# Optimization experiments

Hardware: AMD Instinct MI355X
Metric: run time of the kernel (lower is better)

## Reference

```python
import jax, jax.numpy as jnp
import numpy as np

B = 4096
D = 68 * 68  # 4624
L = 68
E = 1024


def setup_inputs() -> dict:
    key = jax.random.key(0)
    ks = jax.random.split(key, 24)
    rn = lambda k, shape, scale: jax.random.normal(k, shape, dtype=jnp.float32) * scale
    inp = {
        "x": rn(ks[0], (B, D), 1.0),
        "eps": rn(ks[1], (B, L), 1.0),
        # weights scaled ~1/sqrt(fan_in) to avoid sigmoid saturation
        "fc11_w": rn(ks[2], (E, D), 1.0 / np.sqrt(D)),
        "fc11_b": rn(ks[3], (E,), 0.01),
        "fc12_w": rn(ks[4], (E, D), 1.0 / np.sqrt(D)),
        "fc12_b": rn(ks[5], (E,), 0.01),
        "fc21_w": rn(ks[6], (L, E), 1.0 / np.sqrt(E)),
        "fc21_b": rn(ks[7], (L,), 0.01),
        "fc22_w": rn(ks[8], (L, E), 1.0 / np.sqrt(E)),
        "fc22_b": rn(ks[9], (L,), 0.01),
        "W3": rn(ks[10], (5, L, L), 1.0 / np.sqrt(L)),
        "b3": rn(ks[11], (5, L), 0.01),
        "W4": rn(ks[12], (5, L, L), 1.0 / np.sqrt(L)),
        "b4": rn(ks[13], (5, L), 0.01),
        "W5": rn(ks[14], (3, L, L), 1.0 / np.sqrt(L)),
        "b5": rn(ks[15], (3, L), 0.01),
        "fc6_w": rn(ks[16], (D, D), 1.0 / np.sqrt(D)),
        "fc6_b": rn(ks[17], (D,), 0.01),
        "fcy_w": rn(ks[18], (1, L), 1.0 / np.sqrt(L)),
        "fcy_b": rn(ks[19], (1,), 0.01),
    }
    return inp


def _forward(x, eps, fc11_w, fc11_b, fc12_w, fc12_b, fc21_w, fc21_b,
             fc22_w, fc22_b, W3, b3, W4, b4, W5, b5, fc6_w, fc6_b, fcy_w, fcy_b):
    b = x.shape[0]
    # encode (dropout in eval mode -> identity)
    h11 = jax.nn.relu(x @ fc11_w.T + fc11_b)
    h12 = jax.nn.relu(x @ fc12_w.T + fc12_b)
    mu = h11 @ fc21_w.T + fc21_b          # [B, 68]
    logvar = h12 @ fc22_w.T + fc22_b      # [B, 68]
    # reparameterize
    z = mu + eps * jnp.exp(0.5 * logvar)
    y = mu @ fcy_w.T + fcy_b              # [B, 1]
    # decode: 5 parallel 68-dim branches (vectorized over branch axis k)
    h3 = jnp.einsum('bd,kod->kbo', z, W3) + b3[:, None, :]     # [5,B,68]
    # source: h31 has no sigmoid, h32..h35 do
    h3 = jnp.concatenate([h3[:1], jax.nn.sigmoid(h3[1:])], axis=0)
    h4 = jax.nn.sigmoid(jnp.einsum('kbd,kod->kbo', h3, W4) + b4[:, None, :])
    # source reuses fc53 for branches 4 and 5: weight index map [0,1,2,2,2]
    idx = jnp.array([0, 1, 2, 2, 2])
    h5 = jnp.einsum('kbd,kod->kbo', h4, W5[idx]) + b5[idx][:, None, :]  # [5,B,68]
    # source: h6 = h51 only (other branch outer-products are dead code)
    h51 = h5[0]                                                # [B,68]
    outer = (h51[:, :, None] * h51[:, None, :]).reshape(b, D)  # bmm outer product
    recon = jax.nn.sigmoid(outer @ fc6_w.T + fc6_b)            # [B, 4624]
    return recon, mu, logvar, y


def reference(x, eps, fc11_w, fc11_b, fc12_w, fc12_b, fc21_w, fc21_b,
              fc22_w, fc22_b, W3, b3, W4, b4, W5, b5, fc6_w, fc6_b, fcy_w, fcy_b):
    return _forward(x, eps, fc11_w, fc11_b, fc12_w, fc12_b, fc21_w, fc21_b,
                    fc22_w, fc22_b, W3, b3, W4, b4, W5, b5, fc6_w, fc6_b, fcy_w, fcy_b)
```

## Files before the change

### kernel.cpp

```cpp
#include <hip/hip_runtime.h>
#include <hip/hip_bf16.h>
#include <cstdint>
#include <cstddef>

typedef __bf16 bf16x8 __attribute__((ext_vector_type(8)));
typedef __bf16 bf16x4 __attribute__((ext_vector_type(4)));
typedef float  floatx4 __attribute__((ext_vector_type(4)));

#define DEV __device__ __forceinline__

DEV __bf16 f2b(float x) { return (__bf16)x; }

DEV void async_ld16(const void* g, void* l) {
    __builtin_amdgcn_global_load_lds(
        (const __attribute__((address_space(1))) unsigned int*)g,
        (__attribute__((address_space(3))) unsigned int*)l,
        16, 0, 0);
}

#define BATCH 4096
#define DDIM  4624
#define DPAD  4672
#define LDIM  68
#define EDIM  1024
#define N1    2048
#define KB    2048
#define N2PAD 4736
#define NPAIR 2346
#define K2PAD 2368

__global__ void cvt_pad(const float* __restrict__ src, int rows_valid, int K,
                        __bf16* __restrict__ dst, int rows_total) {
    const int gpr = DPAD / 4;
    const long total = (long)rows_total * gpr;
    for (long g = blockIdx.x * (long)blockDim.x + threadIdx.x; g < total;
         g += gridDim.x * (long)blockDim.x) {
        int row = (int)(g / gpr);
        int c4  = (int)(g - (long)row * gpr) * 4;
        bf16x4 v;
        if (row < rows_valid && c4 < K) {
            floatx4 f = *(const floatx4*)(src + (size_t)row * K + c4);
            v[0] = f2b(f[0]); v[1] = f2b(f[1]); v[2] = f2b(f[2]); v[3] = f2b(f[3]);
        } else {
            v[0] = v[1] = v[2] = v[3] = (__bf16)0.0f;
        }
        *(bf16x4*)(dst + (size_t)row * DPAD + c4) = v;
    }
}

__global__ void pad_w2(const float* __restrict__ w21, const float* __restrict__ w22,
                       __bf16* __restrict__ dst) {
    const int total = 144 * 512;
    for (int g = blockIdx.x * blockDim.x + threadIdx.x; g < total;
         g += gridDim.x * blockDim.x) {
        int row = g >> 9;
        int c4  = (g & 511) * 4;
        bf16x4 v;
        v[0] = v[1] = v[2] = v[3] = (__bf16)0.0f;
        if (row < 68 && c4 < 1024) {
            floatx4 f = *(const floatx4*)(w21 + (size_t)row * EDIM + c4);
            v[0] = f2b(f[0]); v[1] = f2b(f[1]); v[2] = f2b(f[2]); v[3] = f2b(f[3]);
        } else if (row >= 68 && row < 136 && c4 >= 1024) {
            floatx4 f = *(const floatx4*)(w22 + (size_t)(row - 68) * EDIM + (c4 - 1024));
            v[0] = f2b(f[0]); v[1] = f2b(f[1]); v[2] = f2b(f[2]); v[3] = f2b(f[3]);
        }
        *(bf16x4*)(dst + (size_t)row * KB + c4) = v;
    }
}

DEV void build_ptab(unsigned short* ptab, int t, int nthr) {
    for (int i = t; i < LDIM; i += nthr) {
        int p0 = i * (137 - i) / 2;
        for (int j = i; j < LDIM; ++j)
            ptab[p0 + (j - i)] = (unsigned short)((i << 8) | j);
    }
}

__global__ void w6sym_build(const float* __restrict__ w6, __bf16* __restrict__ dst) {
    __shared__ float row[DDIM];
    __shared__ unsigned short ptab[K2PAD];
    const int o = blockIdx.x;
    const int t = threadIdx.x;
    if (o < DDIM) {
        const float* src = w6 + (size_t)o * DDIM;
        for (int idx = t; idx < DDIM / 4; idx += 256)
            *(floatx4*)(row + idx * 4) = *(const floatx4*)(src + idx * 4);
    }
    build_ptab(ptab, t, 256);
    __syncthreads();
    for (int p4 = t; p4 < K2PAD / 4; p4 += 256) {
        bf16x4 v;
#pragma unroll
        for (int u = 0; u < 4; ++u) {
            int p = p4 * 4 + u;
            float val = 0.f;
            if (o < DDIM && p < NPAIR) {
                int ij = ptab[p];
                int i = ij >> 8, j = ij & 255;
                val = (i == j) ? row[i * LDIM + i] : (row[i * LDIM + j] + row[j * LDIM + i]);
            }
            v[u] = f2b(val);
        }
        *(bf16x4*)(dst + (size_t)o * K2PAD + p4 * 4) = v;
    }
}

template <int EPI>
__launch_bounds__(256, 2)
__global__ void gemm_bt(const __bf16* __restrict__ A, int lda,
                        const __bf16* __restrict__ W, int ldb, int KT,
                        __bf16* __restrict__ outb, float* __restrict__ outf, int ldc,
                        const float* __restrict__ bias0, const float* __restrict__ bias1) {
    __shared__ __align__(16) __bf16 smA[128 * 64];
    __shared__ __align__(16) __bf16 smB[128 * 64];

    const int t  = threadIdx.x;
    const int l  = t & 63;
    const int w  = t >> 6;
    const int m0 = blockIdx.x * 128;
    const int n0 = blockIdx.y * 128;
    const int wm = (w & 1) * 64;
    const int wn = (w >> 1) * 64;

    const int srow   = t >> 3;
    const int schunk = (t & 7) ^ (srow & 7);
    const __bf16* pa = A + (size_t)(m0 + srow) * lda + schunk * 8;
    const __bf16* pb = W + (size_t)(n0 + srow) * ldb + schunk * 8;
    char* dA = (char*)smA + t * 16;
    char* dB = (char*)smB + t * 16;

    floatx4 acc[4][4];
#pragma unroll
    for (int mi = 0; mi < 4; ++mi)
#pragma unroll
        for (int ni = 0; ni < 4; ++ni) {
            floatx4 z = {0.f, 0.f, 0.f, 0.f};
            acc[mi][ni] = z;
        }

    for (int kt = 0; kt < KT; ++kt) {
#pragma unroll
        for (int i = 0; i < 4; ++i) {
            async_ld16(pa + (size_t)i * 32 * lda, dA + i * 4096);
            async_ld16(pb + (size_t)i * 32 * ldb, dB + i * 4096);
        }
        pa += 64; pb += 64;
        __syncthreads();

#pragma unroll
        for (int h = 0; h < 2; ++h) {
            bf16x8 af[4], bfr[4];
#pragma unroll
            for (int mi = 0; mi < 4; ++mi) {
                int r = wm + mi * 16 + (l & 15);
                int c = ((h << 2) | (l >> 4)) ^ (r & 7);
                af[mi] = *(const bf16x8*)((const char*)smA + r * 128 + c * 16);
            }
#pragma unroll
            for (int ni = 0; ni < 4; ++ni) {
                int r = wn + ni * 16 + (l & 15);
                int c = ((h << 2) | (l >> 4)) ^ (r & 7);
                bfr[ni] = *(const bf16x8*)((const char*)smB + r * 128 + c * 16);
            }
#pragma unroll
            for (int mi = 0; mi < 4; ++mi)
#pragma unroll
                for (int ni = 0; ni < 4; ++ni)
                    acc[mi][ni] = __builtin_amdgcn_mfma_f32_16x16x32_bf16(af[mi], bfr[ni],
                                                                         acc[mi][ni], 0, 0, 0);
        }
        __syncthreads();
    }

    const int colbase = n0 + wn + (l & 15);
    const int rowbase = m0 + wm + (l >> 4) * 4;
#pragma unroll
    for (int ni = 0; ni < 4; ++ni) {
        int col = colbase + ni * 16;
        if (EPI == 1 && col >= DDIM) continue;
        float bias = (EPI == 0)
                         ? ((col < 1024) ? bias0[col] : bias1[col - 1024])
                         : bias0[col];
#pragma unroll
        for (int mi = 0; mi < 4; ++mi) {
            int row = rowbase + mi * 16;
#pragma unroll
            for (int r = 0; r < 4; ++r) {
                float v = acc[mi][ni][r] + bias;
                if (EPI == 0) {
                    v = v > 0.f ? v : 0.f;
                    outb[(size_t)(row + r) * ldc + col] = f2b(v);
                } else {
                    v = 1.f / (1.f + __expf(-v));
                    outf[(size_t)(row + r) * ldc + col] = v;
                }
            }
        }
    }
}

__launch_bounds__(64, 4)
__global__ void gemmB(const __bf16* __restrict__ h, const __bf16* __restrict__ w2,
                      float* __restrict__ muvar) {
    const int l    = threadIdx.x;
    const int m0   = blockIdx.x * 16;
    const int k0   = blockIdx.y * 512;
    const int row  = l & 15;
    const int quad = l >> 4;

    floatx4 acc[9];
#pragma unroll
    for (int ni = 0; ni < 9; ++ni) {
        floatx4 z = {0.f, 0.f, 0.f, 0.f};
        acc[ni] = z;
    }

    const __bf16* ap = h + (size_t)(m0 + row) * KB + k0 + quad * 8;
    for (int kt = 0; kt < 16; ++kt) {
        bf16x8 a = *(const bf16x8*)ap;
        ap += 32;
#pragma unroll
        for (int ni = 0; ni < 9; ++ni) {
            const __bf16* bp = w2 + (size_t)(ni * 16 + row) * KB + k0 + kt * 32 + quad * 8;
            bf16x8 b = *(const bf16x8*)bp;
            acc[ni] = __builtin_amdgcn_mfma_f32_16x16x32_bf16(a, b, acc[ni], 0, 0, 0);
        }
    }
#pragma unroll
    for (int ni = 0; ni < 9; ++ni) {
        int col = ni * 16 + row;
        if (col < 136) {
#pragma unroll
            for (int r = 0; r < 4; ++r) {
                int orow = m0 + quad * 4 + r;
                atomicAdd(&muvar[(size_t)orow * 136 + col], acc[ni][r]);
            }
        }
    }
}

__global__ void decode(const float* __restrict__ muvar, const float* __restrict__ eps,
                       const float* __restrict__ b21, const float* __restrict__ b22,
                       const float* __restrict__ W3, const float* __restrict__ b3,
                       const float* __restrict__ W4, const float* __restrict__ b4,
                       const float* __restrict__ W5, const float* __restrict__ b5,
                       const float* __restrict__ fcyw, const float* __restrict__ fcyb,
                       float* __restrict__ out_mu, float* __restrict__ out_lv,
                       float* __restrict__ out_y, __bf16* __restrict__ A2) {
    __shared__ float w3s[DDIM], w4s[DDIM], w5s[DDIM];
    __shared__ float b3s[LDIM], b4s[LDIM], b5s[LDIM], fys[LDIM];
    __shared__ float zb[16][LDIM], h3b[16][LDIM], h51b[16][LDIM];
    __shared__ unsigned short ptab[K2PAD];

    const int t  = threadIdx.x;
    const int r0 = blockIdx.x * 16;

    for (int i = t; i < DDIM; i += 256) {
        w3s[i] = W3[i];
        w4s[i] = W4[i];
        w5s[i] = W5[i];
    }
    if (t < LDIM) {
        b3s[t] = b3[t];
        b4s[t] = b4[t];
        b5s[t] = b5[t];
        fys[t] = fcyw[t];
    }
    build_ptab(ptab, t, 256);
    __syncthreads();

    for (int idx = t; idx < 16 * LDIM; idx += 256) {
        int r = idx / LDIM, o = idx - r * LDIM;
        int row = r0 + r;
        float mu = muvar[(size_t)row * 136 + o] + b21[o];
        float lv = muvar[(size_t)row * 136 + 68 + o] + b22[o];
        float z  = mu + eps[(size_t)row * LDIM + o] * __expf(0.5f * lv);
        zb[r][o] = z;
        out_mu[(size_t)row * LDIM + o] = mu;
        out_lv[(size_t)row * LDIM + o] = lv;
    }
    if (t < 16) {
        int row = r0 + t;
        float s = fcyb[0];
        for (int o = 0; o < LDIM; ++o)
            s += (muvar[(size_t)row * 136 + o] + b21[o]) * fys[o];
        out_y[row] = s;
    }
    __syncthreads();

    for (int idx = t; idx < 16 * LDIM; idx += 256) {
        int r = idx / LDIM, o = idx - r * LDIM;
        float s = b3s[o];
        for (int d = 0; d < LDIM; ++d) s += zb[r][d] * w3s[o * LDIM + d];
        h3b[r][o] = s;
    }
    __syncthreads();

    for (int idx = t; idx < 16 * LDIM; idx += 256) {
        int r = idx / LDIM, o = idx - r * LDIM;
        float s = b4s[o];
        for (int d = 0; d < LDIM; ++d) s += h3b[r][d] * w4s[o * LDIM + d];
        zb[r][o] = 1.f / (1.f + __expf(-s));
    }
    __syncthreads();

    for (int idx = t; idx < 16 * LDIM; idx += 256) {
        int r = idx / LDIM, o = idx - r * LDIM;
        float s = b5s[o];
        for (int d = 0; d < LDIM; ++d) s += zb[r][d] * w5s[o * LDIM + d];
        h51b[r][o] = s;
    }
    __syncthreads();

    for (int idx = t; idx < 16 * (K2PAD / 4); idx += 256) {
        int r  = idx / (K2PAD / 4);
        int p4 = (idx - r * (K2PAD / 4)) * 4;
        int row = r0 + r;
        bf16x4 v;
#pragma unroll
        for (int u = 0; u < 4; ++u) {
            int p = p4 + u;
            float val = 0.f;
            if (p < NPAIR) {
                int ij = ptab[p];
                val = h51b[r][ij >> 8] * h51b[r][ij & 255];
            }
            v[u] = f2b(val);
        }
        *(bf16x4*)(A2 + (size_t)row * K2PAD + p4) = v;
    }
}

extern "C" void kernel_launch(void* const* d_in, const int* in_sizes, int n_in,
                              void* d_out, int out_size, void* d_ws, size_t ws_size,
                              hipStream_t stream) {
    const float* x    = (const float*)d_in[0];
    const float* eps  = (const float*)d_in[1];
    const float* w11  = (const float*)d_in[2];
    const float* b11  = (const float*)d_in[3];
    const float* w12  = (const float*)d_in[4];
    const float* b12  = (const float*)d_in[5];
    const float* w21  = (const float*)d_in[6];
    const float* b21  = (const float*)d_in[7];
    const float* w22  = (const float*)d_in[8];
    const float* b22  = (const float*)d_in[9];
    const float* W3   = (const float*)d_in[10];
    const float* b3   = (const float*)d_in[11];
    const float* W4   = (const float*)d_in[12];
    const float* b4   = (const float*)d_in[13];
    const float* W5   = (const float*)d_in[14];
    const float* b5   = (const float*)d_in[15];
    const float* w6   = (const float*)d_in[16];
    const float* b6   = (const float*)d_in[17];
    const float* fcyw = (const float*)d_in[18];
    const float* fcyb = (const float*)d_in[19];

    float* out       = (float*)d_out;
    float* out_recon = out;
    float* out_mu    = out + (size_t)BATCH * DDIM;
    float* out_lv    = out_mu + (size_t)BATCH * LDIM;
    float* out_y     = out_lv + (size_t)BATCH * LDIM;

    char* ws = (char*)d_ws;
    size_t off = 0;
    __bf16* xb     = (__bf16*)(ws + off); off += (size_t)BATCH * DPAD * 2;
    __bf16* w1_pad = (__bf16*)(ws + off); off += (size_t)N1 * DPAD * 2;
    __bf16* w6s    = (__bf16*)(ws + off); off += (size_t)N2PAD * K2PAD * 2;
    __bf16* hbuf   = (__bf16*)(ws + off); off += (size_t)BATCH * KB * 2;
    __bf16* w2_pad = (__bf16*)(ws + off); off += (size_t)144 * KB * 2;
    float*  muvar  = (float*) (ws + off); off += (size_t)BATCH * 136 * 4;
    __bf16* A2     = (__bf16*)(ws + off);

    hipMemsetAsync(muvar, 0, (size_t)BATCH * 136 * 4, stream);

    cvt_pad<<<2048, 256, 0, stream>>>(x, BATCH, DDIM, xb, BATCH);
    cvt_pad<<<512, 256, 0, stream>>>(w11, 1024, DDIM, w1_pad, 1024);
    cvt_pad<<<512, 256, 0, stream>>>(w12, 1024, DDIM, w1_pad + (size_t)1024 * DPAD, 1024);
    w6sym_build<<<N2PAD, 256, 0, stream>>>(w6, w6s);
    pad_w2<<<72, 256, 0, stream>>>(w21, w22, w2_pad);

    gemm_bt<0><<<dim3(32, 16), 256, 0, stream>>>(
        xb, DPAD, w1_pad, DPAD, DPAD / 64, hbuf, nullptr, N1, b11, b12);

    gemmB<<<dim3(BATCH / 16, 4), 64, 0, stream>>>(hbuf, w2_pad, muvar);

    decode<<<BATCH / 16, 256, 0, stream>>>(muvar, eps, b21, b22, W3, b3, W4, b4, W5, b5,
                                           fcyw, fcyb, out_mu, out_lv, out_y, A2);

    gemm_bt<1><<<dim3(32, N2PAD / 128), 256, 0, stream>>>(
        A2, K2PAD, w6s, K2PAD, K2PAD / 64, nullptr, out_recon, DDIM, b6, nullptr);
}
```

Baseline: 533.1 us.

## Triple-buffer GEMM K-loop with async prefetch and larger 128x256 tiles

```diff
diff --git a/kernel.cpp b/kernel.cpp
--- a/kernel.cpp
+++ b/kernel.cpp
@@ -20,14 +20,14 @@
 
 #define BATCH 4096
 #define DDIM  4624
-#define DPAD  4672
+#define DPAD  4800
 #define LDIM  68
 #define EDIM  1024
 #define N1    2048
 #define KB    2048
-#define N2PAD 4736
+#define N2PAD 4864
 #define NPAIR 2346
-#define K2PAD 2368
+#define K2PAD 2496
 
 __global__ void cvt_pad(const float* __restrict__ src, int rows_valid, int K,
                         __bf16* __restrict__ dst, int rows_total) {
@@ -106,28 +106,32 @@
 }
 
 template <int EPI>
-__launch_bounds__(256, 2)
+__launch_bounds__(512, 1)
 __global__ void gemm_bt(const __bf16* __restrict__ A, int lda,
                         const __bf16* __restrict__ W, int ldb, int KT,
                         __bf16* __restrict__ outb, float* __restrict__ outf, int ldc,
                         const float* __restrict__ bias0, const float* __restrict__ bias1) {
-    __shared__ __align__(16) __bf16 smA[128 * 64];
-    __shared__ __align__(16) __bf16 smB[128 * 64];
+    __shared__ __align__(16) __bf16 smA[3 * 128 * 64];
+    __shared__ __align__(16) __bf16 smB[3 * 256 * 64];
 
     const int t  = threadIdx.x;
     const int l  = t & 63;
     const int w  = t >> 6;
     const int m0 = blockIdx.x * 128;
-    const int n0 = blockIdx.y * 128;
+    const int n0 = blockIdx.y * 256;
     const int wm = (w & 1) * 64;
     const int wn = (w >> 1) * 64;
 
-    const int srow   = t >> 3;
-    const int schunk = (t & 7) ^ (srow & 7);
-    const __bf16* pa = A + (size_t)(m0 + srow) * lda + schunk * 8;
-    const __bf16* pb = W + (size_t)(n0 + srow) * ldb + schunk * 8;
+    const int lr = t >> 3;
+    const int sw = (t & 7) ^ (lr & 7);
+    const __bf16* pa0 = A + (size_t)(m0 + lr) * lda + sw * 8;
+    const __bf16* pb0 = W + (size_t)(n0 + lr) * ldb + sw * 8;
     char* dA = (char*)smA + t * 16;
     char* dB = (char*)smB + t * 16;
+
+    const int q  = l >> 4;
+    const int ra = wm + (l & 15);
+    const int rb = wn + (l & 15);
 
     floatx4 acc[4][4];
 #pragma unroll
@@ -138,39 +142,65 @@
             acc[mi][ni] = z;
         }
 
-    for (int kt = 0; kt < KT; ++kt) {
-#pragma unroll
-        for (int i = 0; i < 4; ++i) {
-            async_ld16(pa + (size_t)i * 32 * lda, dA + i * 4096);
-            async_ld16(pb + (size_t)i * 32 * ldb, dB + i * 4096);
-        }
-        pa += 64; pb += 64;
-        __syncthreads();
-
+    auto STAGE = [&](int tile, int buf) {
+        const __bf16* sa = pa0 + (size_t)tile * 64;
+        const __bf16* sb = pb0 + (size_t)tile * 64;
+        char* da = dA + buf * 16384;
+        char* db = dB + buf * 32768;
+        async_ld16(sa,                        da);
+        async_ld16(sa + (size_t)64  * lda,    da + 8192);
+        async_ld16(sb,                        db);
+        async_ld16(sb + (size_t)64  * ldb,    db + 8192);
+        async_ld16(sb + (size_t)128 * ldb,    db + 16384);
+        async_ld16(sb + (size_t)192 * ldb,    db + 24576);
+    };
+
+    auto COMPUTE = [&](int ba, int bb) {
+        const char* baseA = (const char*)smA + ba;
+        const char* baseB = (const char*)smB + bb;
 #pragma unroll
         for (int h = 0; h < 2; ++h) {
+            const int c = ((h << 2) | q) ^ (l & 7);
             bf16x8 af[4], bfr[4];
 #pragma unroll
-            for (int mi = 0; mi < 4; ++mi) {
-                int r = wm + mi * 16 + (l & 15);
-                int c = ((h << 2) | (l >> 4)) ^ (r & 7);
-                af[mi] = *(const bf16x8*)((const char*)smA + r * 128 + c * 16);
-            }
-#pragma unroll
-            for (int ni = 0; ni < 4; ++ni) {
-                int r = wn + ni * 16 + (l & 15);
-                int c = ((h << 2) | (l >> 4)) ^ (r & 7);
-                bfr[ni] = *(const bf16x8*)((const char*)smB + r * 128 + c * 16);
-            }
-#pragma unroll
             for (int mi = 0; mi < 4; ++mi)
+                af[mi] = *(const bf16x8*)(baseA + (ra + mi * 16) * 128 + c * 16);
+#pragma unroll
+            for (int ni = 0; ni < 4; ++ni)
+                bfr[ni] = *(const bf16x8*)(baseB + (rb + ni * 16) * 128 + c * 16);
+            __builtin_amdgcn_s_setprio(1);
+#pragma unroll
+            for (int mi = 0; mi < 4; ++mi)
 #pragma unroll
                 for (int ni = 0; ni < 4; ++ni)
-                    acc[mi][ni] = __builtin_amdgcn_mfma_f32_16x16x32_bf16(af[mi], bfr[ni],
-                                                                         acc[mi][ni], 0, 0, 0);
-        }
-        __syncthreads();
-    }
+                    acc[mi][ni] = __builtin_amdgcn_mfma_f32_16x16x32_bf16(
+                        af[mi], bfr[ni], acc[mi][ni], 0, 0, 0);
+            __builtin_amdgcn_s_setprio(0);
+        }
+    };
+
+#define GBODY(BA, BB, DOSTG, STGT, STGBUF, VMS)                         \
+    {                                                                   \
+        asm volatile("s_waitcnt vmcnt(" VMS ")" ::: "memory");          \
+        __builtin_amdgcn_s_barrier();                                   \
+        __builtin_amdgcn_sched_barrier(0);                              \
+        if (DOSTG) STAGE(STGT, STGBUF);                                 \
+        COMPUTE(BA, BB);                                                \
+    }
+
+    STAGE(0, 0);
+    STAGE(1, 1);
+
+    int kt = 0;
+    for (; kt < KT - 3; kt += 3) {
+        GBODY(0,     0,     true, kt + 2, 2, "6");
+        GBODY(16384, 32768, true, kt + 3, 0, "6");
+        GBODY(32768, 65536, true, kt + 4, 1, "6");
+    }
+    GBODY(0,     0,     true,  kt + 2, 2, "6");
+    GBODY(16384, 32768, false, 0,      0, "6");
+    GBODY(32768, 65536, false, 0,      0, "0");
+#undef GBODY
 
     const int colbase = n0 + wn + (l & 15);
     const int rowbase = m0 + wm + (l >> 4) * 4;
@@ -379,7 +409,7 @@
     w6sym_build<<<N2PAD, 256, 0, stream>>>(w6, w6s);
     pad_w2<<<72, 256, 0, stream>>>(w21, w22, w2_pad);
 
-    gemm_bt<0><<<dim3(32, 16), 256, 0, stream>>>(
+    gemm_bt<0><<<dim3(BATCH / 128, N1 / 256), 512, 0, stream>>>(
         xb, DPAD, w1_pad, DPAD, DPAD / 64, hbuf, nullptr, N1, b11, b12);
 
     gemmB<<<dim3(BATCH / 16, 4), 64, 0, stream>>>(hbuf, w2_pad, muvar);
@@ -387,6 +417,6 @@
     decode<<<BATCH / 16, 256, 0, stream>>>(muvar, eps, b21, b22, W3, b3, W4, b4, W5, b5,
                                            fcyw, fcyb, out_mu, out_lv, out_y, A2);
 
-    gemm_bt<1><<<dim3(32, N2PAD / 128), 256, 0, stream>>>(
+    gemm_bt<1><<<dim3(BATCH / 128, N2PAD / 256), 512, 0, stream>>>(
         A2, K2PAD, w6s, K2PAD, K2PAD / 64, nullptr, out_recon, DDIM, b6, nullptr);
 }
```

Result: slower. 560.5 us (+5.1%).
